# Optimization experiments

Hardware: AMD Instinct MI355X
Metric: run time of the kernel (lower is better)

## Reference

```python
import jax, jax.numpy as jnp
import numpy as np

BIG_NUMBER = 1000000.0
B, N, F, D = 8, 256, 128, 128  # batch, nodes, feat dim, mid/out size


def setup_inputs() -> dict:
    key = jax.random.key(0)
    ks = jax.random.split(key, 16)
    node_fts = jax.random.normal(ks[0], (B, N, F), jnp.float32)
    hidden = jax.random.normal(ks[1], (B, N, F), jnp.float32)
    edge_fts = jax.random.normal(ks[2], (B, N, N, F), jnp.float32)
    e_hidden = jax.random.normal(ks[3], (B, N, N, F), jnp.float32)
    graph_fts = jax.random.normal(ks[4], (B, F), jnp.float32)
    adj_mat = jax.random.randint(ks[5], (B, N, N), 0, 2, jnp.int32)
    s = 0.05
    We = jax.random.normal(ks[6], (2 * F, D), jnp.float32) * s
    be = jnp.zeros((D,), jnp.float32)
    W_m1 = jax.random.normal(ks[7], (2 * F, D), jnp.float32) * s
    b_m1 = jnp.zeros((D,), jnp.float32)
    W_m2 = jax.random.normal(ks[8], (2 * F, D), jnp.float32) * s
    b_m2 = jnp.zeros((D,), jnp.float32)
    W_o1 = jax.random.normal(ks[9], (2 * F, D), jnp.float32) * s
    b_o1 = jnp.zeros((D,), jnp.float32)
    W_o2 = jax.random.normal(ks[10], (D, D), jnp.float32) * s
    b_o2 = jnp.zeros((D,), jnp.float32)
    return dict(node_fts=node_fts, edge_fts=edge_fts, graph_fts=graph_fts,
                adj_mat=adj_mat, hidden=hidden, e_hidden=e_hidden,
                We=We, be=be, W_m1=W_m1, b_m1=b_m1, W_m2=W_m2, b_m2=b_m2,
                W_o1=W_o1, b_o1=b_o1, W_o2=W_o2, b_o2=b_o2)


def reference(node_fts, edge_fts, graph_fts, adj_mat, hidden, e_hidden,
              We, be, W_m1, b_m1, W_m2, b_m2, W_o1, b_o1, W_o2, b_o2):
    # concat node/edge feats with hiddens
    nt = jnp.concatenate([node_fts, hidden], axis=-1)            # [B,N,2F]
    et = jnp.concatenate([edge_fts, e_hidden], axis=-1) @ We + be  # [B,N,N,D]
    # append virtual node (zeros features, fully connected)
    nt = jnp.concatenate([nt, jnp.zeros((B, 1, 2 * F), nt.dtype)], axis=1)  # [B,N+1,2F]
    adj = adj_mat.astype(nt.dtype)
    adj = jnp.concatenate([adj, jnp.ones((B, 1, N), nt.dtype)], axis=1)
    adj = jnp.concatenate([adj, jnp.ones((B, N + 1, 1), nt.dtype)], axis=2)  # [B,N+1,N+1]
    # MPNN layer (reduction = max)
    msg_1 = nt @ W_m1 + b_m1  # [B,N+1,D]
    msg_2 = nt @ W_m2 + b_m2  # [B,N+1,D]
    msgs = msg_1[:, None, :, :] + msg_2[:, :, None, :]  # [B,N+1,N+1,D]
    msgs = jnp.where(adj[..., None] > 0, msgs, -BIG_NUMBER)
    msgs = jnp.max(msgs, axis=1)  # [B,N+1,D]
    ret = (nt @ W_o1 + b_o1) + (msgs @ W_o2 + b_o2)  # [B,N+1,D]
    # strip virtual node; padded edge tensor sliced back equals et
    return ret[:, :N, :], et
```

## Files before the change

### kernel.cpp

```cpp
#include <hip/hip_runtime.h>
#include <hip/hip_bf16.h>

#define Bn 8
#define Nn 256
#define Fn 128
#define Dn 128

typedef __bf16 bf16_t;
typedef bf16_t bf16x8 __attribute__((ext_vector_type(8)));
typedef bf16_t bf16x4 __attribute__((ext_vector_type(4)));
typedef float f32x4 __attribute__((ext_vector_type(4)));

#define GLOAD16(g, l) __builtin_amdgcn_global_load_lds(                        \
    (const __attribute__((address_space(1))) void*)(g),                        \
    (__attribute__((address_space(3))) void*)(l), 16, 0, 0)

__global__ __launch_bounds__(1024, 4) void mfma_gemm_kernel(
    const float* __restrict__ edge, const float* __restrict__ ehid,
    const float* __restrict__ We,   const float* __restrict__ be,
    const float* __restrict__ node, const float* __restrict__ hidden,
    const float* __restrict__ W_m1, const float* __restrict__ b_m1,
    const float* __restrict__ W_m2, const float* __restrict__ b_m2,
    const float* __restrict__ W_o1, const float* __restrict__ b_o1,
    float* __restrict__ out_et,
    float* __restrict__ ws_m1, float* __restrict__ ws_m2, float* __restrict__ ws_h1)
{
    __shared__ __align__(16) char smem[131072];
    bf16_t* wlds = (bf16_t*)smem;
    float*  albs = (float*)(smem + 65536);

    const int t = threadIdx.x;

    const float *X1, *X2, *W, *bias;
    float* out;
    long rowbase;
    bool streaming;
    if (blockIdx.x >= 24) {
        X1 = edge; X2 = ehid; W = We; bias = be; out = out_et;
        rowbase = (long)(blockIdx.x - 24) * 256;
        streaming = true;
    } else {
        const int e = blockIdx.x;
        const int w = e >> 3;
        rowbase = (long)(e & 7) * 256;
        X1 = node; X2 = hidden; streaming = false;
        if (w == 0)      { W = W_m2; bias = b_m2; out = ws_m2; }
        else if (w == 1) { W = W_m1; bias = b_m1; out = ws_m1; }
        else             { W = W_o1; bias = b_o1; out = ws_h1; }
    }

    const int wv     = t >> 6;
    const int l      = t & 63;
    const int lane16 = l & 15;
    const int quad   = l >> 4;

    const long wrow = rowbase + wv * 16;

    const int arow0 = l >> 3;
    const int akg   = (l & 7) ^ (arow0 & 7);
    const float* aX1 = X1 + (wrow + arow0) * 128 + akg * 4;
    const float* aX2 = X2 + (wrow + arow0) * 128 + akg * 4;
    float* abw = albs + wv * 1024;

#define ISSUE_CHUNK(c_, b_) do {                                              \
        const float* s_ = ((c_) < 4) ? (aX1 + (c_) * 32)                      \
                                     : (aX2 + ((c_) - 4) * 32);               \
        float* d_ = abw + (b_) * 512;                                         \
        GLOAD16(s_,        d_);                                               \
        GLOAD16(s_ + 1024, d_ + 256);             \
    } while (0)

    ISSUE_CHUNK(0, 0);
    ISSUE_CHUNK(1, 1);

    {
        const int kb4 = t >> 4;
        const int g   = t & 15;
        const int k0  = kb4 * 4;
        const float* wp = W + (long)k0 * 128 + g * 8;
        f32x4 a0[4], a1[4];
        #pragma unroll
        for (int r = 0; r < 4; ++r) {
            a0[r] = *(const f32x4*)(wp + r * 128);
            a1[r] = *(const f32x4*)(wp + r * 128 + 4);
        }
        #pragma unroll
        for (int j = 0; j < 8; ++j) {
            const int n  = g * 8 + j;
            const int cp = (kb4 >> 1) ^ j ^ (g & 7);
            bf16x4 v;
            #pragma unroll
            for (int r = 0; r < 4; ++r)
                v[r] = (bf16_t)(j < 4 ? a0[r][j] : a1[r][j - 4]);
            *(bf16x4*)(&wlds[n * 256 + cp * 8 + (k0 & 7)]) = v;
        }
    }
    __syncthreads();

    float bev[8];
    #pragma unroll
    for (int nt = 0; nt < 8; ++nt) bev[nt] = bias[nt * 16 + lane16];

    f32x4 acc[8];
    #pragma unroll
    for (int nt = 0; nt < 8; ++nt) acc[nt] = (f32x4){0.f, 0.f, 0.f, 0.f};

    const int kst0 = (quad * 2)     ^ (lane16 & 7);
    const int kst1 = (quad * 2 + 1) ^ (lane16 & 7);

    #pragma unroll
    for (int c = 0; c < 8; ++c) {
        const int b = c & 1;

        if (c < 7) asm volatile("s_waitcnt vmcnt(2)" ::: "memory");
        else       asm volatile("s_waitcnt vmcnt(0)" ::: "memory");
        __builtin_amdgcn_sched_barrier(0);

        const float* bufp = abw + b * 512 + lane16 * 32;
        f32x4 u0 = *(const f32x4*)(bufp + kst0 * 4);
        f32x4 u1 = *(const f32x4*)(bufp + kst1 * 4);
        bf16x8 afrag;
        #pragma unroll
        for (int j = 0; j < 4; ++j) {
            afrag[j]     = (bf16_t)u0[j];
            afrag[j + 4] = (bf16_t)u1[j];
        }

        asm volatile("s_waitcnt lgkmcnt(0)" ::: "memory");
        __builtin_amdgcn_sched_barrier(0);
        if (c + 2 < 8) ISSUE_CHUNK(c + 2, b);

        #pragma unroll
        for (int nt = 0; nt < 8; ++nt) {
            const int n    = nt * 16 + lane16;
            const int cidx = c * 4 + quad;
            const int cp   = cidx ^ (n & 7) ^ ((n >> 3) & 7);
            bf16x8 bfrag = *(const bf16x8*)(&wlds[n * 256 + cp * 8]);
            acc[nt] = __builtin_amdgcn_mfma_f32_16x16x32_bf16(afrag, bfrag, acc[nt], 0, 0, 0);
        }
    }
#undef ISSUE_CHUNK

    const long orow0 = wrow + quad * 4;
    #pragma unroll
    for (int nt = 0; nt < 8; ++nt) {
        #pragma unroll
        for (int r = 0; r < 4; ++r) {
            const float v = acc[nt][r] + bev[nt];
            float* p = out + (orow0 + r) * 128 + nt * 16 + lane16;
            if (streaming) __builtin_nontemporal_store(v, p);
            else           *p = v;
        }
    }
}

__global__ __launch_bounds__(256) void ret_kernel(
    const int* __restrict__ adj,
    const float* __restrict__ m2, const float* __restrict__ m1,
    const float* __restrict__ h1,
    const float* __restrict__ W_o2, const float* __restrict__ b_o2,
    const float* __restrict__ b_m2,
    float* __restrict__ out)
{
    __shared__ int   adjc[256];
    __shared__ float part[8][128];
    __shared__ float sv[128];

    const int bj = blockIdx.x;
    const int b  = bj >> 8;
    const int j  = bj & 255;
    const int t  = threadIdx.x;

    adjc[t] = adj[(b * 256 + t) * 256 + j];
    __syncthreads();

    const int s  = t >> 5;
    const int dg = t & 31;
    f32x4 mx4;
    mx4[0] = mx4[1] = mx4[2] = mx4[3] = -3.0e38f;
    const float* m2p = m2 + ((long)b * 256 + s * 32) * 128 + dg * 4;
    #pragma unroll 8
    for (int i = 0; i < 32; ++i) {
        const f32x4 v = *(const f32x4*)(m2p + i * 128);
        const bool on = (adjc[s * 32 + i] != 0);
        mx4[0] = on ? fmaxf(mx4[0], v[0]) : mx4[0];
        mx4[1] = on ? fmaxf(mx4[1], v[1]) : mx4[1];
        mx4[2] = on ? fmaxf(mx4[2], v[2]) : mx4[2];
        mx4[3] = on ? fmaxf(mx4[3], v[3]) : mx4[3];
    }
    *(f32x4*)&part[s][dg * 4] = mx4;
    __syncthreads();

    if (t < 128) {
        float m = b_m2[t];
        #pragma unroll
        for (int ss = 0; ss < 8; ++ss) m = fmaxf(m, part[ss][t]);
        sv[t] = m1[bj * 128 + t] + m;
    }
    __syncthreads();

    const int d = t & 127;
    const int h = t >> 7;
    float r = 0.f;
    const float* wp = W_o2 + (h * 64) * 128 + d;
    #pragma unroll 8
    for (int k = 0; k < 64; ++k)
        r += sv[h * 64 + k] * wp[k * 128];

    if (h == 1) part[0][d] = r;
    __syncthreads();
    if (h == 0)
        out[bj * 128 + d] = r + part[0][d] + h1[bj * 128 + d] + b_o2[d];
}

extern "C" void kernel_launch(void* const* d_in, const int* in_sizes, int n_in,
                              void* d_out, int out_size, void* d_ws, size_t ws_size,
                              hipStream_t stream)
{
    const float* node   = (const float*)d_in[0];
    const float* edge   = (const float*)d_in[1];
    const int*   adj    = (const int*)d_in[3];
    const float* hidden = (const float*)d_in[4];
    const float* ehid   = (const float*)d_in[5];
    const float* We     = (const float*)d_in[6];
    const float* be     = (const float*)d_in[7];
    const float* W_m1   = (const float*)d_in[8];
    const float* b_m1   = (const float*)d_in[9];
    const float* W_m2   = (const float*)d_in[10];
    const float* b_m2   = (const float*)d_in[11];
    const float* W_o1   = (const float*)d_in[12];
    const float* b_o1   = (const float*)d_in[13];
    const float* W_o2   = (const float*)d_in[14];
    const float* b_o2   = (const float*)d_in[15];

    float* out_ret = (float*)d_out;
    float* out_et  = (float*)d_out + Bn * Nn * Dn;

    float* ws_m2 = (float*)d_ws;
    float* ws_m1 = ws_m2 + 2048 * 128;
    float* ws_h1 = ws_m1 + 2048 * 128;

    hipLaunchKernelGGL(mfma_gemm_kernel, dim3(2048 + 24), dim3(1024), 0, stream,
                       edge, ehid, We, be, node, hidden,
                       W_m1, b_m1, W_m2, b_m2, W_o1, b_o1,
                       out_et, ws_m1, ws_m2, ws_h1);
    hipLaunchKernelGGL(ret_kernel, dim3(2048), dim3(256), 0, stream,
                       adj, ws_m2, ws_m1, ws_h1, W_o2, b_o2, b_m2, out_ret);
}
```

Baseline: 643.4 us.

## Make GEMM blocks persistent over four row tiles to amortize weight staging

```diff
diff --git a/kernel.cpp b/kernel.cpp
--- a/kernel.cpp
+++ b/kernel.cpp
@@ -33,16 +33,16 @@
 
     const float *X1, *X2, *W, *bias;
     float* out;
-    long rowbase;
+    long rowbase0;
     bool streaming;
-    if (blockIdx.x >= 24) {
+    if (blockIdx.x >= 6) {
         X1 = edge; X2 = ehid; W = We; bias = be; out = out_et;
-        rowbase = (long)(blockIdx.x - 24) * 256;
+        rowbase0 = (long)(blockIdx.x - 6) * 1024;
         streaming = true;
     } else {
         const int e = blockIdx.x;
-        const int w = e >> 3;
-        rowbase = (long)(e & 7) * 256;
+        const int w = e >> 1;
+        rowbase0 = (long)(e & 1) * 1024;
         X1 = node; X2 = hidden; streaming = false;
         if (w == 0)      { W = W_m2; bias = b_m2; out = ws_m2; }
         else if (w == 1) { W = W_m1; bias = b_m1; out = ws_m1; }
@@ -54,24 +54,25 @@
     const int lane16 = l & 15;
     const int quad   = l >> 4;
 
-    const long wrow = rowbase + wv * 16;
-
     const int arow0 = l >> 3;
     const int akg   = (l & 7) ^ (arow0 & 7);
-    const float* aX1 = X1 + (wrow + arow0) * 128 + akg * 4;
-    const float* aX2 = X2 + (wrow + arow0) * 128 + akg * 4;
+    const long laneoff = ((long)(wv * 16 + arow0)) * 128 + akg * 4;
+    const float* aX1 = X1 + rowbase0 * 128 + laneoff;
+    const float* aX2 = X2 + rowbase0 * 128 + laneoff;
     float* abw = albs + wv * 1024;
 
-#define ISSUE_CHUNK(c_, b_) do {                                              \
-        const float* s_ = ((c_) < 4) ? (aX1 + (c_) * 32)                      \
-                                     : (aX2 + ((c_) - 4) * 32);               \
+    const long TSTR = 256 * 128;
+
+#define ISSUE_CHUNK(x1, x2, c_, b_) do {                                      \
+        const float* s_ = ((c_) < 4) ? ((x1) + (c_) * 32)                     \
+                                     : ((x2) + ((c_) - 4) * 32);              \
         float* d_ = abw + (b_) * 512;                                         \
         GLOAD16(s_,        d_);                                               \
-        GLOAD16(s_ + 1024, d_ + 256);             \
+        GLOAD16(s_ + 1024, d_ + 256);            \
     } while (0)
 
-    ISSUE_CHUNK(0, 0);
-    ISSUE_CHUNK(1, 1);
+    ISSUE_CHUNK(aX1, aX2, 0, 0);
+    ISSUE_CHUNK(aX1, aX2, 1, 1);
 
     {
         const int kb4 = t >> 4;
@@ -101,57 +102,66 @@
     #pragma unroll
     for (int nt = 0; nt < 8; ++nt) bev[nt] = bias[nt * 16 + lane16];
 
-    f32x4 acc[8];
-    #pragma unroll
-    for (int nt = 0; nt < 8; ++nt) acc[nt] = (f32x4){0.f, 0.f, 0.f, 0.f};
-
     const int kst0 = (quad * 2)     ^ (lane16 & 7);
     const int kst1 = (quad * 2 + 1) ^ (lane16 & 7);
 
-    #pragma unroll
-    for (int c = 0; c < 8; ++c) {
-        const int b = c & 1;
-
-        if (c < 7) asm volatile("s_waitcnt vmcnt(2)" ::: "memory");
-        else       asm volatile("s_waitcnt vmcnt(0)" ::: "memory");
-        __builtin_amdgcn_sched_barrier(0);
-
-        const float* bufp = abw + b * 512 + lane16 * 32;
-        f32x4 u0 = *(const f32x4*)(bufp + kst0 * 4);
-        f32x4 u1 = *(const f32x4*)(bufp + kst1 * 4);
-        bf16x8 afrag;
-        #pragma unroll
-        for (int j = 0; j < 4; ++j) {
-            afrag[j]     = (bf16_t)u0[j];
-            afrag[j + 4] = (bf16_t)u1[j];
-        }
-
-        asm volatile("s_waitcnt lgkmcnt(0)" ::: "memory");
-        __builtin_amdgcn_sched_barrier(0);
-        if (c + 2 < 8) ISSUE_CHUNK(c + 2, b);
-
+    for (int tile = 0; tile < 4; ++tile) {
+        const float* cX1 = aX1 + tile * TSTR;
+        const float* cX2 = aX2 + tile * TSTR;
+        const float* nX1 = cX1 + TSTR;
+        const float* nX2 = cX2 + TSTR;
+        const bool   lastt = (tile == 3);
+
+        f32x4 acc[8];
+        #pragma unroll
+        for (int nt = 0; nt < 8; ++nt) acc[nt] = (f32x4){0.f, 0.f, 0.f, 0.f};
+
+        #pragma unroll
+        for (int c = 0; c < 8; ++c) {
+            const int b = c & 1;
+
+            if (lastt && c == 7) asm volatile("s_waitcnt vmcnt(0)" ::: "memory");
+            else                 asm volatile("s_waitcnt vmcnt(2)" ::: "memory");
+            __builtin_amdgcn_sched_barrier(0);
+
+            const float* bufp = abw + b * 512 + lane16 * 32;
+            f32x4 u0 = *(const f32x4*)(bufp + kst0 * 4);
+            f32x4 u1 = *(const f32x4*)(bufp + kst1 * 4);
+            bf16x8 afrag;
+            #pragma unroll
+            for (int j = 0; j < 4; ++j) {
+                afrag[j]     = (bf16_t)u0[j];
+                afrag[j + 4] = (bf16_t)u1[j];
+            }
+
+            asm volatile("s_waitcnt lgkmcnt(0)" ::: "memory");
+            __builtin_amdgcn_sched_barrier(0);
+            if (c < 6)        ISSUE_CHUNK(cX1, cX2, c + 2, b);
+            else if (!lastt)  ISSUE_CHUNK(nX1, nX2, c - 6, b);
+
+            #pragma unroll
+            for (int nt = 0; nt < 8; ++nt) {
+                const int n    = nt * 16 + lane16;
+                const int cidx = c * 4 + quad;
+                const int cp   = cidx ^ (n & 7) ^ ((n >> 3) & 7);
+                bf16x8 bfrag = *(const bf16x8*)(&wlds[n * 256 + cp * 8]);
+                acc[nt] = __builtin_amdgcn_mfma_f32_16x16x32_bf16(afrag, bfrag, acc[nt], 0, 0, 0);
+            }
+        }
+
+        const long orow0 = rowbase0 + tile * 256 + wv * 16 + quad * 4;
         #pragma unroll
         for (int nt = 0; nt < 8; ++nt) {
-            const int n    = nt * 16 + lane16;
-            const int cidx = c * 4 + quad;
-            const int cp   = cidx ^ (n & 7) ^ ((n >> 3) & 7);
-            bf16x8 bfrag = *(const bf16x8*)(&wlds[n * 256 + cp * 8]);
-            acc[nt] = __builtin_amdgcn_mfma_f32_16x16x32_bf16(afrag, bfrag, acc[nt], 0, 0, 0);
+            #pragma unroll
+            for (int r = 0; r < 4; ++r) {
+                const float v = acc[nt][r] + bev[nt];
+                float* p = out + (orow0 + r) * 128 + nt * 16 + lane16;
+                if (streaming) __builtin_nontemporal_store(v, p);
+                else           *p = v;
+            }
         }
     }
 #undef ISSUE_CHUNK
-
-    const long orow0 = wrow + quad * 4;
-    #pragma unroll
-    for (int nt = 0; nt < 8; ++nt) {
-        #pragma unroll
-        for (int r = 0; r < 4; ++r) {
-            const float v = acc[nt][r] + bev[nt];
-            float* p = out + (orow0 + r) * 128 + nt * 16 + lane16;
-            if (streaming) __builtin_nontemporal_store(v, p);
-            else           *p = v;
-        }
-    }
 }
 
 __global__ __launch_bounds__(256) void ret_kernel(
@@ -240,7 +250,7 @@
     float* ws_m1 = ws_m2 + 2048 * 128;
     float* ws_h1 = ws_m1 + 2048 * 128;
 
-    hipLaunchKernelGGL(mfma_gemm_kernel, dim3(2048 + 24), dim3(1024), 0, stream,
+    hipLaunchKernelGGL(mfma_gemm_kernel, dim3(518), dim3(1024), 0, stream,
                        edge, ehid, We, be, node, hidden,
                        W_m1, b_m1, W_m2, b_m2, W_o1, b_o1,
                        out_et, ws_m1, ws_m2, ws_h1);
```

After: 680.8 us. 1.06x slower.
